# Optimization experiments

Hardware: AMD Instinct MI355X
Metric: run time of the kernel (lower is better)

Reference implementation:

```python
import jax, jax.numpy as jnp
import numpy as np

D_MODEL = 1024
N_HEAD = 16
D_HEAD = D_MODEL // N_HEAD
B, S = 4, 2048


def setup_inputs() -> dict:
    key = jax.random.key(0)
    ks = jax.random.split(key, 10)
    def xavier(k, shape):
        fan_in, fan_out = shape[1], shape[0]
        limit = np.sqrt(6.0 / (fan_in + fan_out))
        return jax.random.uniform(k, shape, jnp.float32, -limit, limit)
    x = jax.random.normal(ks[0], (B, S, D_MODEL), jnp.float32)
    mask = jnp.tril(jnp.ones((S, S), jnp.int32))[None, None]  # causal [1,1,S,S]
    return {
        "x": x,
        "Wq": xavier(ks[1], (D_MODEL, D_MODEL)), "bq": jnp.zeros((D_MODEL,), jnp.float32),
        "Wk": xavier(ks[2], (D_MODEL, D_MODEL)), "bk": jnp.zeros((D_MODEL,), jnp.float32),
        "Wv": xavier(ks[3], (D_MODEL, D_MODEL)), "bv": jnp.zeros((D_MODEL,), jnp.float32),
        "Wo": xavier(ks[4], (D_MODEL, D_MODEL)), "bo": jnp.zeros((D_MODEL,), jnp.float32),
        "mask": mask,
    }


def reference(x, Wq, bq, Wk, bk, Wv, bv, Wo, bo, mask):
    b, s, d = x.shape
    # Linear layers use y = x @ W.T + b (torch convention)
    def proj(W, bias):
        y = jnp.einsum('bsd,ed->bse', x, W) + bias
        return y.reshape(b, s, N_HEAD, D_HEAD).transpose(0, 2, 1, 3)  # [B,H,S,Dh]
    q = proj(Wq, bq)
    k = proj(Wk, bk)
    v = proj(Wv, bv)
    scores = jnp.einsum('bhqd,bhkd->bhqk', q, k) / jnp.sqrt(jnp.float32(D_HEAD))
    scores = jnp.where(mask == 0, jnp.float32(-1e9), scores)
    attn = jax.nn.softmax(scores, axis=-1)  # dropout is identity at eval
    context = jnp.einsum('bhqk,bhkd->bhqd', attn, v)
    context = context.transpose(0, 2, 1, 3).reshape(b, s, d)
    return jnp.einsum('bsd,ed->bse', context, Wo) + bo
```

## Files before the change

### kernel.cpp

```cpp
#include <hip/hip_runtime.h>
#include <stdint.h>

#define D_MODEL 1024
#define NHEAD   16
#define DHEAD   64
#define BATCH   4
#define SEQ     2048
#define MTOT    (BATCH*SEQ)

typedef __attribute__((ext_vector_type(4))) float f32x4;
typedef __attribute__((ext_vector_type(8))) short bf16x8;

typedef __attribute__((address_space(3))) uint32_t lds_u32;
typedef const __attribute__((address_space(1))) uint32_t glb_u32;

__device__ static inline void gload_lds16(const void* g, void* l) {
    __builtin_amdgcn_global_load_lds((glb_u32*)g, (lds_u32*)l, 16, 0, 0);
}

__device__ static inline ushort f2bf(float f) {
    uint32_t u = __builtin_bit_cast(uint32_t, f);
    u += 0x7fffu + ((u >> 16) & 1u);
    return (ushort)(u >> 16);
}

__device__ static inline float exp2_fast(float x) {
    float r; asm("v_exp_f32 %0, %1" : "=v"(r) : "v"(x)); return r;
}
__device__ static inline uint32_t cvt_pk_bf16(float a, float b) {
    uint32_t r;
    asm("v_cvt_pk_bf16_f32 %0, %1, %2" : "=v"(r) : "v"(a), "v"(b));
    return r;
}

__global__ __launch_bounds__(256) void convert_kernel(
    const float4* __restrict__ x,
    const float4* __restrict__ wq, const float4* __restrict__ wk,
    const float4* __restrict__ wv, const float4* __restrict__ wo,
    ushort4* __restrict__ xb, ushort4* __restrict__ wb)
{
    const int NX4 = (MTOT * D_MODEL) / 4;
    const int NW4 = (D_MODEL * D_MODEL) / 4;
    const int TOT = NX4 + 4 * NW4;
    for (int i = blockIdx.x * blockDim.x + threadIdx.x; i < TOT;
         i += gridDim.x * blockDim.x) {
        float4 v; ushort4* dst;
        if (i < NX4) { v = x[i]; dst = &xb[i]; }
        else {
            int j = i - NX4;
            int w = j >> 18;
            int r = j & (NW4 - 1);
            const float4* s = (w == 0) ? wq : (w == 1) ? wk : (w == 2) ? wv : wo;
            v = s[r]; dst = &wb[(size_t)w * NW4 + r];
        }
        ushort4 o;
        o.x = f2bf(v.x); o.y = f2bf(v.y); o.z = f2bf(v.z); o.w = f2bf(v.w);
        *dst = o;
    }
}

template<int LAYOUT>
__global__ __launch_bounds__(256) void gemm_bt(
    const ushort* __restrict__ A,
    const ushort* __restrict__ W,
    const float*  __restrict__ bias,
    void* __restrict__ out, float scale)
{
    __shared__ __align__(16) ushort As[128 * 32];
    __shared__ __align__(16) ushort Bs[128 * 32];

    const int tid = threadIdx.x;
    const int w  = tid >> 6, l = tid & 63, lo = l & 15, hi = l >> 4;
    const int wr = w >> 1, wc = w & 1;

    const int id = blockIdx.y * 8 + blockIdx.x;
    const int mb = ((id & 7) << 3) | ((id >> 3) & 7);
    const int nb = id >> 6;
    const int m0 = mb * 128, n0 = nb * 128;

    f32x4 acc[4][4] = {};

    const int srow = l >> 2;
    const int sk   = (l & 3) * 8;

    for (int kt = 0; kt < 32; ++kt) {
        const int k0 = kt * 32;
        __syncthreads();
#pragma unroll
        for (int c = 0; c < 2; ++c) {
            const int row = c * 64 + w * 16 + srow;
            gload_lds16(&A[(size_t)(m0 + row) * 1024 + k0 + sk],
                        &As[(c * 64 + w * 16) * 32]);
            gload_lds16(&W[(size_t)(n0 + row) * 1024 + k0 + sk],
                        &Bs[(c * 64 + w * 16) * 32]);
        }
        __syncthreads();

        bf16x8 af[4], bfr[4];
#pragma unroll
        for (int mi = 0; mi < 4; ++mi)
            af[mi] = *(const bf16x8*)&As[(wr * 64 + mi * 16 + lo) * 32 + hi * 8];
#pragma unroll
        for (int ni = 0; ni < 4; ++ni)
            bfr[ni] = *(const bf16x8*)&Bs[(wc * 64 + ni * 16 + lo) * 32 + hi * 8];
#pragma unroll
        for (int mi = 0; mi < 4; ++mi)
#pragma unroll
            for (int ni = 0; ni < 4; ++ni)
                acc[mi][ni] = __builtin_amdgcn_mfma_f32_16x16x32_bf16(
                    af[mi], bfr[ni], acc[mi][ni], 0, 0, 0);
    }

#pragma unroll
    for (int mi = 0; mi < 4; ++mi) {
#pragma unroll
        for (int ni = 0; ni < 4; ++ni) {
            const int gj = n0 + wc * 64 + ni * 16 + lo;
            const float bj = bias[gj];
            if (LAYOUT == 0) {
#pragma unroll
                for (int r = 0; r < 4; ++r) {
                    const int gi = m0 + wr * 64 + mi * 16 + hi * 4 + r;
                    const int b = gi >> 11, s = gi & (SEQ - 1);
                    const int h = gj >> 6, dh = gj & 63;
                    ((ushort*)out)[(((size_t)(b * NHEAD + h)) * SEQ + s) * DHEAD + dh] =
                        f2bf((acc[mi][ni][r] + bj) * scale);
                }
            } else if (LAYOUT == 1) {
                const int gi0 = m0 + wr * 64 + mi * 16 + hi * 4;
                const int b = gi0 >> 11, s = gi0 & (SEQ - 1);
                const int h = gj >> 6, dh = gj & 63;
                ushort4 o4;
                o4.x = f2bf((acc[mi][ni][0] + bj) * scale);
                o4.y = f2bf((acc[mi][ni][1] + bj) * scale);
                o4.z = f2bf((acc[mi][ni][2] + bj) * scale);
                o4.w = f2bf((acc[mi][ni][3] + bj) * scale);
                *(ushort4*)&((ushort*)out)[(((size_t)(b * NHEAD + h)) * DHEAD + dh) * SEQ + s] = o4;
            } else {
#pragma unroll
                for (int r = 0; r < 4; ++r) {
                    const int gi = m0 + wr * 64 + mi * 16 + hi * 4 + r;
                    ((float*)out)[(size_t)gi * D_MODEL + gj] = (acc[mi][ni][r] + bj) * scale;
                }
            }
        }
    }
}

__global__ __launch_bounds__(256) void attn_kernel(
    const ushort* __restrict__ Q, const ushort* __restrict__ K,
    const ushort* __restrict__ Vt, ushort* __restrict__ ctx)
{
    __shared__ __align__(16) ushort Ks[64 * 64];
    __shared__ __align__(16) ushort Vs[64 * 64];
    __shared__ __align__(16) ushort Pq[4 * 32 * 64];

    const int tid = threadIdx.x;
    const int w = tid >> 6, l = tid & 63, lo = l & 15, hi = l >> 4;
    const int sw = lo & 7;

    const int fid = blockIdx.x;
    const int xcd = fid & 7;
    const int u = fid >> 3;
    const int g = xcd * 8 + (u & 7);
    const int b = g >> 4, h = g & 15;
    const int j = u >> 3;
    const size_t base = (size_t)(b * NHEAD + h) * SEQ * DHEAD;

    const int krow = tid >> 3;
    const int kcol = (tid & 7) * 8;
    char* PqW = (char*)&Pq[w * 2048];

    for (int pass = 0; pass < 2; ++pass) {
        const int qt = pass ? (15 - j) : j;
        const int q0 = qt << 7;
        const int qw0 = q0 + w * 32;

        bf16x8 qf[2][2];
#pragma unroll
        for (int mi = 0; mi < 2; ++mi)
#pragma unroll
            for (int ks = 0; ks < 2; ++ks)
                qf[mi][ks] = *(const bf16x8*)&Q[base +
                    (size_t)(qw0 + mi * 16 + lo) * DHEAD + ks * 32 + hi * 8];

        f32x4 o[2][4] = {};
        float mrow[2] = {-1e30f, -1e30f}, lrow[2] = {0.f, 0.f};

        const int ntiles = (q0 + 128) >> 6;
        bf16x8 kreg[2], vreg[2];
#pragma unroll
        for (int c = 0; c < 2; ++c) {
            kreg[c] = *(const bf16x8*)&K[base + (size_t)(c * 32 + krow) * DHEAD + kcol];
            vreg[c] = *(const bf16x8*)&Vt[base + (size_t)(c * 32 + krow) * SEQ + kcol];
        }

        for (int t = 0; t < ntiles; ++t) {
            const int kv0 = t << 6;
            __syncthreads();
#pragma unroll
            for (int c = 0; c < 2; ++c) {
                const int row = c * 32 + krow;
                const int g16 = (tid & 7) ^ (row & 7);
                *(bf16x8*)((char*)Ks + row * 128 + (g16 << 4)) = kreg[c];
                *(bf16x8*)((char*)Vs + row * 128 + (g16 << 4)) = vreg[c];
            }
            __syncthreads();
            if (t + 1 < ntiles) {
                const int nv0 = kv0 + 64;
#pragma unroll
                for (int c = 0; c < 2; ++c) {
                    kreg[c] = *(const bf16x8*)&K[base + (size_t)(nv0 + c * 32 + krow) * DHEAD + kcol];
                    vreg[c] = *(const bf16x8*)&Vt[base + (size_t)(c * 32 + krow) * SEQ + nv0 + kcol];
                }
            }
            if (kv0 > qw0 + 31) continue;

            f32x4 s[2][4] = {};
#pragma unroll
            for (int ks = 0; ks < 2; ++ks) {
                bf16x8 kf[4];
#pragma unroll
                for (int nj = 0; nj < 4; ++nj)
                    kf[nj] = *(const bf16x8*)((char*)Ks + (nj * 16 + lo) * 128 +
                                              ((((ks << 2) + hi) ^ sw) << 4));
#pragma unroll
                for (int mi = 0; mi < 2; ++mi)
#pragma unroll
                    for (int nj = 0; nj < 4; ++nj)
                        s[mi][nj] = __builtin_amdgcn_mfma_f32_16x16x32_bf16(
                            kf[nj], qf[mi][ks], s[mi][nj], 0, 0, 0);
            }

            if (kv0 + 63 > qw0) {
#pragma unroll
                for (int mi = 0; mi < 2; ++mi) {
                    const int gq = qw0 + mi * 16 + lo;
#pragma unroll
                    for (int nj = 0; nj < 4; ++nj)
#pragma unroll
                        for (int r = 0; r < 4; ++r) {
                            const int gk = kv0 + nj * 16 + hi * 4 + r;
                            if (gk > gq) s[mi][nj][r] = -1e30f;
                        }
                }
            }

            float tl[2], corr[2];
#pragma unroll
            for (int mi = 0; mi < 2; ++mi) {
                float m = s[mi][0][0];
#pragma unroll
                for (int nj = 0; nj < 4; ++nj)
#pragma unroll
                    for (int r = 0; r < 4; ++r) m = fmaxf(m, s[mi][nj][r]);
                tl[mi] = m;
            }
            const bool grow = (tl[0] > mrow[0] + 8.f) | (tl[1] > mrow[1] + 8.f);
            if (__any(grow)) {
#pragma unroll
                for (int mi = 0; mi < 2; ++mi) {
                    float m2 = fmaxf(tl[mi], __shfl_xor(tl[mi], 16));
                    m2 = fmaxf(m2, __shfl_xor(m2, 32));
                    const float mn = fmaxf(mrow[mi], m2);
                    corr[mi] = exp2_fast(mrow[mi] - mn);
                    mrow[mi] = mn;
                }
#pragma unroll
                for (int mi = 0; mi < 2; ++mi)
#pragma unroll
                    for (int r = 0; r < 4; ++r) {
                        const float cb = __shfl(corr[mi], hi * 4 + r);
#pragma unroll
                        for (int ni = 0; ni < 4; ++ni) o[mi][ni][r] *= cb;
                    }
            } else { corr[0] = 1.f; corr[1] = 1.f; }

#pragma unroll
            for (int mi = 0; mi < 2; ++mi) {
                float ls = 0.f;
#pragma unroll
                for (int nj = 0; nj < 4; ++nj) {
#pragma unroll
                    for (int r = 0; r < 4; ++r) {
                        const float p = exp2_fast(s[mi][nj][r] - mrow[mi]);
                        s[mi][nj][r] = p;
                        ls += p;
                    }
                    uint2 pp;
                    pp.x = cvt_pk_bf16(s[mi][nj][0], s[mi][nj][1]);
                    pp.y = cvt_pk_bf16(s[mi][nj][2], s[mi][nj][3]);
                    const int gP = ((nj << 1) + (hi >> 1)) ^ sw;
                    *(uint2*)(PqW + (mi * 16 + lo) * 128 + (gP << 4) + ((hi & 1) << 3)) = pp;
                }
                ls += __shfl_xor(ls, 16);
                ls += __shfl_xor(ls, 32);
                lrow[mi] = lrow[mi] * corr[mi] + ls;
            }

#pragma unroll
            for (int ks2 = 0; ks2 < 2; ++ks2) {
                bf16x8 pf[2], vf[4];
#pragma unroll
                for (int mi = 0; mi < 2; ++mi)
                    pf[mi] = *(const bf16x8*)(PqW + (mi * 16 + lo) * 128 +
                                              ((((ks2 << 2) + hi) ^ sw) << 4));
#pragma unroll
                for (int ni = 0; ni < 4; ++ni)
                    vf[ni] = *(const bf16x8*)((char*)Vs + (ni * 16 + lo) * 128 +
                                              ((((ks2 << 2) + hi) ^ sw) << 4));
#pragma unroll
                for (int mi = 0; mi < 2; ++mi)
#pragma unroll
                    for (int ni = 0; ni < 4; ++ni)
                        o[mi][ni] = __builtin_amdgcn_mfma_f32_16x16x32_bf16(
                            pf[mi], vf[ni], o[mi][ni], 0, 0, 0);
            }
        }

#pragma unroll
        for (int mi = 0; mi < 2; ++mi) {
            const float rv = 1.0f / lrow[mi];
#pragma unroll
            for (int r = 0; r < 4; ++r) {
                const float rb = __shfl(rv, hi * 4 + r);
                const int gq = qw0 + mi * 16 + hi * 4 + r;
#pragma unroll
                for (int ni = 0; ni < 4; ++ni)
                    ctx[((size_t)(b * SEQ + gq)) * D_MODEL + h * DHEAD + ni * 16 + lo] =
                        f2bf(o[mi][ni][r] * rb);
            }
        }
    }
}

extern "C" void kernel_launch(void* const* d_in, const int* in_sizes, int n_in,
                              void* d_out, int out_size, void* d_ws, size_t ws_size,
                              hipStream_t stream) {
    const float* x  = (const float*)d_in[0];
    const float* Wq = (const float*)d_in[1];
    const float* bq = (const float*)d_in[2];
    const float* Wk = (const float*)d_in[3];
    const float* bk = (const float*)d_in[4];
    const float* Wv = (const float*)d_in[5];
    const float* bv = (const float*)d_in[6];
    const float* Wo = (const float*)d_in[7];
    const float* bo = (const float*)d_in[8];

    char* ws = (char*)d_ws;
    ushort* xb  = (ushort*)(ws);
    ushort* wb  = (ushort*)(ws + (16u << 20));
    ushort* Qb  = (ushort*)(ws + (24u << 20));
    ushort* Kb  = (ushort*)(ws + (40u << 20));
    ushort* Vtb = (ushort*)(ws + (56u << 20));
    ushort* ctx = (ushort*)(ws + (72u << 20));

    convert_kernel<<<2048, 256, 0, stream>>>(
        (const float4*)x, (const float4*)Wq, (const float4*)Wk,
        (const float4*)Wv, (const float4*)Wo, (ushort4*)xb, (ushort4*)wb);

    const int NW = D_MODEL * D_MODEL;
    dim3 ggrid(D_MODEL / 128, MTOT / 128);
    const float qscale = 0.125f * 1.44269504f;
    gemm_bt<0><<<ggrid, 256, 0, stream>>>(xb, wb + 0 * NW, bq, Qb, qscale);
    gemm_bt<0><<<ggrid, 256, 0, stream>>>(xb, wb + 1 * NW, bk, Kb, 1.0f);
    gemm_bt<1><<<ggrid, 256, 0, stream>>>(xb, wb + 2 * NW, bv, Vtb, 1.0f);

    attn_kernel<<<512, 256, 0, stream>>>(Qb, Kb, Vtb, ctx);

    gemm_bt<2><<<ggrid, 256, 0, stream>>>(ctx, wb + 3 * NW, bo, (float*)d_out, 1.0f);
}
```

Baseline: 184.5 us.

## Fuse QKV projections into one launch and halve attention query tile per wave

Merges the three Q/K/V projection GEMMs into a single 1536-block kernel that picks bias, scale and output layout per N-region. This removes two launches and the tail gaps between them. The attention kernel now gives each wave 16 query rows instead of 32 and uses 64-row query tiles with 1024 blocks, which doubles parallelism and cuts per-wave registers. It also adds s_setprio around the MFMA sections. The trade-off is that each K/V tile loaded into LDS is reused by fewer query rows, so global and LDS traffic per unit of work increases.

```diff
diff --git a/kernel.cpp b/kernel.cpp
--- a/kernel.cpp
+++ b/kernel.cpp
@@ -59,12 +59,98 @@
     }
 }
 
-template<int LAYOUT>
-__global__ __launch_bounds__(256) void gemm_bt(
+__global__ __launch_bounds__(256) void gemm_qkv(
+    const ushort* __restrict__ A,
+    const ushort* __restrict__ W3,
+    const float* __restrict__ bq, const float* __restrict__ bk,
+    const float* __restrict__ bv,
+    ushort* __restrict__ Qb, ushort* __restrict__ Kb, ushort* __restrict__ Vtb,
+    float qscale)
+{
+    __shared__ __align__(16) ushort As[128 * 32];
+    __shared__ __align__(16) ushort Bs[128 * 32];
+
+    const int tid = threadIdx.x;
+    const int w  = tid >> 6, l = tid & 63, lo = l & 15, hi = l >> 4;
+    const int wr = w >> 1, wc = w & 1;
+
+    const int id = blockIdx.x;
+    const int mb = ((id & 7) << 3) | ((id >> 3) & 7);
+    const int nb = id >> 6;
+    const int m0 = mb * 128, n0 = nb * 128;
+
+    f32x4 acc[4][4] = {};
+    const int srow = l >> 2;
+    const int sk   = (l & 3) * 8;
+
+    for (int kt = 0; kt < 32; ++kt) {
+        const int k0 = kt * 32;
+        __syncthreads();
+#pragma unroll
+        for (int c = 0; c < 2; ++c) {
+            const int row = c * 64 + w * 16 + srow;
+            gload_lds16(&A[(size_t)(m0 + row) * 1024 + k0 + sk],
+                        &As[(c * 64 + w * 16) * 32]);
+            gload_lds16(&W3[(size_t)(n0 + row) * 1024 + k0 + sk],
+                        &Bs[(c * 64 + w * 16) * 32]);
+        }
+        __syncthreads();
+
+        bf16x8 af[4], bfr[4];
+#pragma unroll
+        for (int mi = 0; mi < 4; ++mi)
+            af[mi] = *(const bf16x8*)&As[(wr * 64 + mi * 16 + lo) * 32 + hi * 8];
+#pragma unroll
+        for (int ni = 0; ni < 4; ++ni)
+            bfr[ni] = *(const bf16x8*)&Bs[(wc * 64 + ni * 16 + lo) * 32 + hi * 8];
+#pragma unroll
+        for (int mi = 0; mi < 4; ++mi)
+#pragma unroll
+            for (int ni = 0; ni < 4; ++ni)
+                acc[mi][ni] = __builtin_amdgcn_mfma_f32_16x16x32_bf16(
+                    af[mi], bfr[ni], acc[mi][ni], 0, 0, 0);
+    }
+
+    const int region = nb >> 3;
+    const float scale = (region == 0) ? qscale : 1.0f;
+    const float* bias = (region == 0) ? bq : (region == 1) ? bk : bv;
+    ushort* outQK = (region == 0) ? Qb : Kb;
+
+#pragma unroll
+    for (int mi = 0; mi < 4; ++mi) {
+#pragma unroll
+        for (int ni = 0; ni < 4; ++ni) {
+            const int gj  = n0 + wc * 64 + ni * 16 + lo;
+            const int lcl = gj & 1023;
+            const int h = lcl >> 6, dh = lcl & 63;
+            const float bj = bias[lcl];
+            if (region < 2) {
+#pragma unroll
+                for (int r = 0; r < 4; ++r) {
+                    const int gi = m0 + wr * 64 + mi * 16 + hi * 4 + r;
+                    const int b = gi >> 11, s = gi & (SEQ - 1);
+                    outQK[(((size_t)(b * NHEAD + h)) * SEQ + s) * DHEAD + dh] =
+                        f2bf((acc[mi][ni][r] + bj) * scale);
+                }
+            } else {
+                const int gi0 = m0 + wr * 64 + mi * 16 + hi * 4;
+                const int b = gi0 >> 11, s = gi0 & (SEQ - 1);
+                ushort4 o4;
+                o4.x = f2bf(acc[mi][ni][0] + bj);
+                o4.y = f2bf(acc[mi][ni][1] + bj);
+                o4.z = f2bf(acc[mi][ni][2] + bj);
+                o4.w = f2bf(acc[mi][ni][3] + bj);
+                *(ushort4*)&Vtb[(((size_t)(b * NHEAD + h)) * DHEAD + dh) * SEQ + s] = o4;
+            }
+        }
+    }
+}
+
+__global__ __launch_bounds__(256) void gemm_out(
     const ushort* __restrict__ A,
     const ushort* __restrict__ W,
     const float*  __restrict__ bias,
-    void* __restrict__ out, float scale)
+    float* __restrict__ out)
 {
     __shared__ __align__(16) ushort As[128 * 32];
     __shared__ __align__(16) ushort Bs[128 * 32];
@@ -79,7 +165,6 @@
     const int m0 = mb * 128, n0 = nb * 128;
 
     f32x4 acc[4][4] = {};
-
     const int srow = l >> 2;
     const int sk   = (l & 3) * 8;
 
@@ -112,39 +197,17 @@
     }
 
 #pragma unroll
-    for (int mi = 0; mi < 4; ++mi) {
+    for (int mi = 0; mi < 4; ++mi)
 #pragma unroll
         for (int ni = 0; ni < 4; ++ni) {
             const int gj = n0 + wc * 64 + ni * 16 + lo;
             const float bj = bias[gj];
-            if (LAYOUT == 0) {
-#pragma unroll
-                for (int r = 0; r < 4; ++r) {
-                    const int gi = m0 + wr * 64 + mi * 16 + hi * 4 + r;
-                    const int b = gi >> 11, s = gi & (SEQ - 1);
-                    const int h = gj >> 6, dh = gj & 63;
-                    ((ushort*)out)[(((size_t)(b * NHEAD + h)) * SEQ + s) * DHEAD + dh] =
-                        f2bf((acc[mi][ni][r] + bj) * scale);
-                }
-            } else if (LAYOUT == 1) {
-                const int gi0 = m0 + wr * 64 + mi * 16 + hi * 4;
-                const int b = gi0 >> 11, s = gi0 & (SEQ - 1);
-                const int h = gj >> 6, dh = gj & 63;
-                ushort4 o4;
-                o4.x = f2bf((acc[mi][ni][0] + bj) * scale);
-                o4.y = f2bf((acc[mi][ni][1] + bj) * scale);
-                o4.z = f2bf((acc[mi][ni][2] + bj) * scale);
-                o4.w = f2bf((acc[mi][ni][3] + bj) * scale);
-                *(ushort4*)&((ushort*)out)[(((size_t)(b * NHEAD + h)) * DHEAD + dh) * SEQ + s] = o4;
-            } else {
-#pragma unroll
-                for (int r = 0; r < 4; ++r) {
-                    const int gi = m0 + wr * 64 + mi * 16 + hi * 4 + r;
-                    ((float*)out)[(size_t)gi * D_MODEL + gj] = (acc[mi][ni][r] + bj) * scale;
-                }
-            }
-        }
-    }
+#pragma unroll
+            for (int r = 0; r < 4; ++r) {
+                const int gi = m0 + wr * 64 + mi * 16 + hi * 4 + r;
+                out[(size_t)gi * D_MODEL + gj] = acc[mi][ni][r] + bj;
+            }
+        }
 }
 
 __global__ __launch_bounds__(256) void attn_kernel(
@@ -153,7 +216,7 @@
 {
     __shared__ __align__(16) ushort Ks[64 * 64];
     __shared__ __align__(16) ushort Vs[64 * 64];
-    __shared__ __align__(16) ushort Pq[4 * 32 * 64];
+    __shared__ __align__(16) ushort Pq[4 * 16 * 64];
 
     const int tid = threadIdx.x;
     const int w = tid >> 6, l = tid & 63, lo = l & 15, hi = l >> 4;
@@ -169,25 +232,23 @@
 
     const int krow = tid >> 3;
     const int kcol = (tid & 7) * 8;
-    char* PqW = (char*)&Pq[w * 2048];
+    char* PqW = (char*)&Pq[w * 1024];
 
     for (int pass = 0; pass < 2; ++pass) {
-        const int qt = pass ? (15 - j) : j;
-        const int q0 = qt << 7;
-        const int qw0 = q0 + w * 32;
-
-        bf16x8 qf[2][2];
-#pragma unroll
-        for (int mi = 0; mi < 2; ++mi)
-#pragma unroll
-            for (int ks = 0; ks < 2; ++ks)
-                qf[mi][ks] = *(const bf16x8*)&Q[base +
-                    (size_t)(qw0 + mi * 16 + lo) * DHEAD + ks * 32 + hi * 8];
-
-        f32x4 o[2][4] = {};
-        float mrow[2] = {-1e30f, -1e30f}, lrow[2] = {0.f, 0.f};
-
-        const int ntiles = (q0 + 128) >> 6;
+        const int qt = pass ? (31 - j) : j;
+        const int q0 = qt << 6;
+        const int qw0 = q0 + w * 16;
+
+        bf16x8 qf[2];
+#pragma unroll
+        for (int ks = 0; ks < 2; ++ks)
+            qf[ks] = *(const bf16x8*)&Q[base +
+                (size_t)(qw0 + lo) * DHEAD + ks * 32 + hi * 8];
+
+        f32x4 o[4] = {};
+        float mrow = -1e30f, lrow = 0.f;
+
+        const int ntiles = qt + 1;
         bf16x8 kreg[2], vreg[2];
 #pragma unroll
         for (int c = 0; c < 2; ++c) {
@@ -214,9 +275,10 @@
                     vreg[c] = *(const bf16x8*)&Vt[base + (size_t)(c * 32 + krow) * SEQ + nv0 + kcol];
                 }
             }
-            if (kv0 > qw0 + 31) continue;
-
-            f32x4 s[2][4] = {};
+            if (kv0 > qw0 + 15) continue;
+
+            f32x4 s[4] = {};
+            __builtin_amdgcn_s_setprio(1);
 #pragma unroll
             for (int ks = 0; ks < 2; ++ks) {
                 bf16x8 kf[4];
@@ -225,111 +287,89 @@
                     kf[nj] = *(const bf16x8*)((char*)Ks + (nj * 16 + lo) * 128 +
                                               ((((ks << 2) + hi) ^ sw) << 4));
 #pragma unroll
-                for (int mi = 0; mi < 2; ++mi)
-#pragma unroll
-                    for (int nj = 0; nj < 4; ++nj)
-                        s[mi][nj] = __builtin_amdgcn_mfma_f32_16x16x32_bf16(
-                            kf[nj], qf[mi][ks], s[mi][nj], 0, 0, 0);
-            }
+                for (int nj = 0; nj < 4; ++nj)
+                    s[nj] = __builtin_amdgcn_mfma_f32_16x16x32_bf16(
+                        kf[nj], qf[ks], s[nj], 0, 0, 0);
+            }
+            __builtin_amdgcn_s_setprio(0);
 
             if (kv0 + 63 > qw0) {
-#pragma unroll
-                for (int mi = 0; mi < 2; ++mi) {
-                    const int gq = qw0 + mi * 16 + lo;
-#pragma unroll
-                    for (int nj = 0; nj < 4; ++nj)
-#pragma unroll
-                        for (int r = 0; r < 4; ++r) {
-                            const int gk = kv0 + nj * 16 + hi * 4 + r;
-                            if (gk > gq) s[mi][nj][r] = -1e30f;
-                        }
+                const int gq = qw0 + lo;
+#pragma unroll
+                for (int nj = 0; nj < 4; ++nj)
+#pragma unroll
+                    for (int r = 0; r < 4; ++r) {
+                        const int gk = kv0 + nj * 16 + hi * 4 + r;
+                        if (gk > gq) s[nj][r] = -1e30f;
+                    }
+            }
+
+            float tl = s[0][0];
+#pragma unroll
+            for (int nj = 0; nj < 4; ++nj)
+#pragma unroll
+                for (int r = 0; r < 4; ++r) tl = fmaxf(tl, s[nj][r]);
+            float corr = 1.f;
+            if (__any(tl > mrow + 8.f)) {
+                float m2 = fmaxf(tl, __shfl_xor(tl, 16));
+                m2 = fmaxf(m2, __shfl_xor(m2, 32));
+                const float mn = fmaxf(mrow, m2);
+                corr = exp2_fast(mrow - mn);
+                mrow = mn;
+#pragma unroll
+                for (int r = 0; r < 4; ++r) {
+                    const float cb = __shfl(corr, hi * 4 + r);
+#pragma unroll
+                    for (int ni = 0; ni < 4; ++ni) o[ni][r] *= cb;
                 }
             }
 
-            float tl[2], corr[2];
-#pragma unroll
-            for (int mi = 0; mi < 2; ++mi) {
-                float m = s[mi][0][0];
-#pragma unroll
-                for (int nj = 0; nj < 4; ++nj)
-#pragma unroll
-                    for (int r = 0; r < 4; ++r) m = fmaxf(m, s[mi][nj][r]);
-                tl[mi] = m;
-            }
-            const bool grow = (tl[0] > mrow[0] + 8.f) | (tl[1] > mrow[1] + 8.f);
-            if (__any(grow)) {
-#pragma unroll
-                for (int mi = 0; mi < 2; ++mi) {
-                    float m2 = fmaxf(tl[mi], __shfl_xor(tl[mi], 16));
-                    m2 = fmaxf(m2, __shfl_xor(m2, 32));
-                    const float mn = fmaxf(mrow[mi], m2);
-                    corr[mi] = exp2_fast(mrow[mi] - mn);
-                    mrow[mi] = mn;
+            float ls = 0.f;
+#pragma unroll
+            for (int nj = 0; nj < 4; ++nj) {
+#pragma unroll
+                for (int r = 0; r < 4; ++r) {
+                    const float p = exp2_fast(s[nj][r] - mrow);
+                    s[nj][r] = p;
+                    ls += p;
                 }
-#pragma unroll
-                for (int mi = 0; mi < 2; ++mi)
-#pragma unroll
-                    for (int r = 0; r < 4; ++r) {
-                        const float cb = __shfl(corr[mi], hi * 4 + r);
-#pragma unroll
-                        for (int ni = 0; ni < 4; ++ni) o[mi][ni][r] *= cb;
-                    }
-            } else { corr[0] = 1.f; corr[1] = 1.f; }
-
-#pragma unroll
-            for (int mi = 0; mi < 2; ++mi) {
-                float ls = 0.f;
-#pragma unroll
-                for (int nj = 0; nj < 4; ++nj) {
-#pragma unroll
-                    for (int r = 0; r < 4; ++r) {
-                        const float p = exp2_fast(s[mi][nj][r] - mrow[mi]);
-                        s[mi][nj][r] = p;
-                        ls += p;
-                    }
-                    uint2 pp;
-                    pp.x = cvt_pk_bf16(s[mi][nj][0], s[mi][nj][1]);
-                    pp.y = cvt_pk_bf16(s[mi][nj][2], s[mi][nj][3]);
-                    const int gP = ((nj << 1) + (hi >> 1)) ^ sw;
-                    *(uint2*)(PqW + (mi * 16 + lo) * 128 + (gP << 4) + ((hi & 1) << 3)) = pp;
-                }
-                ls += __shfl_xor(ls, 16);
-                ls += __shfl_xor(ls, 32);
-                lrow[mi] = lrow[mi] * corr[mi] + ls;
-            }
-
+                uint2 pp;
+                pp.x = cvt_pk_bf16(s[nj][0], s[nj][1]);
+                pp.y = cvt_pk_bf16(s[nj][2], s[nj][3]);
+                const int gP = ((nj << 1) + (hi >> 1)) ^ sw;
+                *(uint2*)(PqW + lo * 128 + (gP << 4) + ((hi & 1) << 3)) = pp;
+            }
+            ls += __shfl_xor(ls, 16);
+            ls += __shfl_xor(ls, 32);
+            lrow = lrow * corr + ls;
+
+            __builtin_amdgcn_s_setprio(1);
 #pragma unroll
             for (int ks2 = 0; ks2 < 2; ++ks2) {
-                bf16x8 pf[2], vf[4];
-#pragma unroll
-                for (int mi = 0; mi < 2; ++mi)
-                    pf[mi] = *(const bf16x8*)(PqW + (mi * 16 + lo) * 128 +
-                                              ((((ks2 << 2) + hi) ^ sw) << 4));
+                bf16x8 pf, vf[4];
+                pf = *(const bf16x8*)(PqW + lo * 128 +
+                                      ((((ks2 << 2) + hi) ^ sw) << 4));
 #pragma unroll
                 for (int ni = 0; ni < 4; ++ni)
                     vf[ni] = *(const bf16x8*)((char*)Vs + (ni * 16 + lo) * 128 +
                                               ((((ks2 << 2) + hi) ^ sw) << 4));
 #pragma unroll
-                for (int mi = 0; mi < 2; ++mi)
-#pragma unroll
-                    for (int ni = 0; ni < 4; ++ni)
-                        o[mi][ni] = __builtin_amdgcn_mfma_f32_16x16x32_bf16(
-                            pf[mi], vf[ni], o[mi][ni], 0, 0, 0);
-            }
-        }
-
-#pragma unroll
-        for (int mi = 0; mi < 2; ++mi) {
-            const float rv = 1.0f / lrow[mi];
-#pragma unroll
-            for (int r = 0; r < 4; ++r) {
-                const float rb = __shfl(rv, hi * 4 + r);
-                const int gq = qw0 + mi * 16 + hi * 4 + r;
-#pragma unroll
                 for (int ni = 0; ni < 4; ++ni)
-                    ctx[((size_t)(b * SEQ + gq)) * D_MODEL + h * DHEAD + ni * 16 + lo] =
-                        f2bf(o[mi][ni][r] * rb);
-            }
+                    o[ni] = __builtin_amdgcn_mfma_f32_16x16x32_bf16(
+                        pf, vf[ni], o[ni], 0, 0, 0);
+            }
+            __builtin_amdgcn_s_setprio(0);
+        }
+
+        const float rv = 1.0f / lrow;
+#pragma unroll
+        for (int r = 0; r < 4; ++r) {
+            const float rb = __shfl(rv, hi * 4 + r);
+            const int gq = qw0 + hi * 4 + r;
+#pragma unroll
+            for (int ni = 0; ni < 4; ++ni)
+                ctx[((size_t)(b * SEQ + gq)) * D_MODEL + h * DHEAD + ni * 16 + lo] =
+                    f2bf(o[ni][r] * rb);
         }
     }
 }
@@ -360,13 +400,11 @@
         (const float4*)Wv, (const float4*)Wo, (ushort4*)xb, (ushort4*)wb);
 
     const int NW = D_MODEL * D_MODEL;
-    dim3 ggrid(D_MODEL / 128, MTOT / 128);
     const float qscale = 0.125f * 1.44269504f;
-    gemm_bt<0><<<ggrid, 256, 0, stream>>>(xb, wb + 0 * NW, bq, Qb, qscale);
-    gemm_bt<0><<<ggrid, 256, 0, stream>>>(xb, wb + 1 * NW, bk, Kb, 1.0f);
-    gemm_bt<1><<<ggrid, 256, 0, stream>>>(xb, wb + 2 * NW, bv, Vtb, 1.0f);
-
-    attn_kernel<<<512, 256, 0, stream>>>(Qb, Kb, Vtb, ctx);
-
-    gemm_bt<2><<<ggrid, 256, 0, stream>>>(ctx, wb + 3 * NW, bo, (float*)d_out, 1.0f);
-}
+
+    gemm_qkv<<<1536, 256, 0, stream>>>(xb, wb, bq, bk, bv, Qb, Kb, Vtb, qscale);
+
+    attn_kernel<<<1024, 256, 0, stream>>>(Qb, Kb, Vtb, ctx);
+
+    gemm_out<<<dim3(8, 64), 256, 0, stream>>>(ctx, wb + 3 * NW, bo, (float*)d_out);
+}
```

Measured after the change: 189.0 us. 2.5% more time.
